# Kernel tuning notes

Measured on AMD Instinct MI355X. Metric: run time of the kernel, lower is better.

The kernel has to match this reference:

```python
import jax, jax.numpy as jnp
import numpy as np

B, N, D = 2, 2048, 1024
H = 16
HD = D // H  # head_dim = 64
EPS = 1e-5


def _layernorm(x, gamma, beta):
    mu = jnp.mean(x, axis=-1, keepdims=True)
    var = jnp.var(x, axis=-1, keepdims=True)
    return (x - mu) * jax.lax.rsqrt(var + EPS) * gamma + beta


def setup_inputs() -> dict:
    key = jax.random.key(0)
    ks = jax.random.split(key, 13)
    s = 1.0 / np.sqrt(D)
    return {
        "query": jax.random.normal(ks[0], (B, N, D), dtype=jnp.float32),
        "Wq": jax.random.uniform(ks[1], (D, D), jnp.float32, -s, s),
        "bq": jax.random.uniform(ks[2], (D,), jnp.float32, -s, s),
        "Wk": jax.random.uniform(ks[3], (D, D), jnp.float32, -s, s),
        "bk": jax.random.uniform(ks[4], (D,), jnp.float32, -s, s),
        "Wv": jax.random.uniform(ks[5], (D, D), jnp.float32, -s, s),
        "bv": jax.random.uniform(ks[6], (D,), jnp.float32, -s, s),
        "Wp": jax.random.uniform(ks[7], (D, D), jnp.float32, -s, s),
        "bp": jax.random.uniform(ks[8], (D,), jnp.float32, -s, s),
        "q_gamma": jnp.ones((HD,), jnp.float32),
        "q_beta": jnp.zeros((HD,), jnp.float32),
        "k_gamma": jnp.ones((HD,), jnp.float32),
        "k_beta": jnp.zeros((HD,), jnp.float32),
    }


def reference(query, Wq, bq, Wk, bk, Wv, bv, Wp, bp, q_gamma, q_beta, k_gamma, k_beta):
    # Linear projections (torch Linear: x @ W.T + b)
    def split_heads(x):  # [B,N,D] -> [B,H,N,HD]
        return x.reshape(B, N, H, HD).transpose(0, 2, 1, 3)

    Q = split_heads(query @ Wq.T + bq)
    K = split_heads(query @ Wk.T + bk)
    V = split_heads(query @ Wv.T + bv)

    # per-head QK LayerNorm
    Q = _layernorm(Q, q_gamma, q_beta)
    K = _layernorm(K, k_gamma, k_beta)

    scale = 1.0 / np.sqrt(HD)
    attn = jax.nn.softmax(jnp.einsum('bhqd,bhkd->bhqk', Q, K) * scale, axis=-1)
    # dropout_prob = 0.0 -> identity
    out = jnp.einsum('bhqk,bhkd->bqhd', attn, V).reshape(B, N, D)
    return out @ Wp.T + bp
```

## Files before the change

kernel.cpp:

```cpp
#include <hip/hip_runtime.h>
#include <math.h>

#define Bb 2
#define Nn 2048
#define Dd 1024
#define Hh 16
#define HD 64

typedef __attribute__((ext_vector_type(8))) short short8;
typedef __attribute__((ext_vector_type(4))) short short4v;
typedef __attribute__((ext_vector_type(4))) float floatx4;

__device__ __forceinline__ short f2bf(float x) {
    unsigned u = __float_as_uint(x);
    u += 0x7fffu + ((u >> 16) & 1u);
    return (short)(u >> 16);
}

#if defined(__has_builtin)
#  if __has_builtin(__builtin_amdgcn_mfma_f32_16x16x16bf16_1k)
#    define MFMA16(a, b, c) __builtin_amdgcn_mfma_f32_16x16x16bf16_1k(a, b, c, 0, 0, 0)
#  endif
#endif
#ifndef MFMA16
static __device__ __forceinline__ floatx4 mfma16_asm(short4v a, short4v b, floatx4 c) {
    asm volatile("v_mfma_f32_16x16x16_bf16 %0, %1, %2, %0" : "+v"(c) : "v"(a), "v"(b));
    return c;
}
#  define MFMA16(a, b, c) mfma16_asm(a, b, c)
#endif

__device__ __forceinline__ void gload16(const void* g, void* l) {
    __builtin_amdgcn_global_load_lds(
        (const __attribute__((address_space(1))) unsigned int*)g,
        (__attribute__((address_space(3))) unsigned int*)l,
        16, 0, 0);
}

#define QSCALE 0.18033688011112042f

__global__ __launch_bounds__(256) void cast_all(
    const float* __restrict__ x,
    const float* __restrict__ Wq, const float* __restrict__ Wk,
    const float* __restrict__ Wv, const float* __restrict__ Wp,
    short* __restrict__ xh, short* __restrict__ Wqh, short* __restrict__ Wkh,
    short* __restrict__ Wvh, short* __restrict__ Wph)
{
    const float* src; short* dst; int n4;
    switch (blockIdx.y) {
        case 0:  src = x;  dst = xh;  n4 = (Bb * Nn * Dd) / 4; break;
        case 1:  src = Wq; dst = Wqh; n4 = (Dd * Dd) / 4; break;
        case 2:  src = Wk; dst = Wkh; n4 = (Dd * Dd) / 4; break;
        case 3:  src = Wv; dst = Wvh; n4 = (Dd * Dd) / 4; break;
        default: src = Wp; dst = Wph; n4 = (Dd * Dd) / 4; break;
    }
    const int i = blockIdx.x * 256 + threadIdx.x;
    if (i >= n4) return;
    float4 v = ((const float4*)src)[i];
    short4v o;
    o.x = f2bf(v.x); o.y = f2bf(v.y); o.z = f2bf(v.z); o.w = f2bf(v.w);
    ((short4v*)dst)[i] = o;
}

__global__ __launch_bounds__(256) void qkv_ln_gemm(
    const short* __restrict__ xh,
    const short* __restrict__ Wqh, const short* __restrict__ Wkh,
    const short* __restrict__ Wvh,
    const float* __restrict__ bq, const float* __restrict__ bk,
    const float* __restrict__ bv,
    const float* __restrict__ qg, const float* __restrict__ qb,
    const float* __restrict__ kg, const float* __restrict__ kb,
    short* __restrict__ Qh, short* __restrict__ Kh, short* __restrict__ Vt)
{
    const int z = blockIdx.z;
    const short* A; const short* W;
    int rowBase, colBase, Nc;
    if (z < 2) { A = xh;  W = z ? Wkh : Wqh;
                 rowBase = blockIdx.x * 128; colBase = blockIdx.y * 128; Nc = Dd; }
    else       { A = Wvh; W = xh;
                 rowBase = blockIdx.y * 128; colBase = blockIdx.x * 128; Nc = Bb * Nn; }

    __shared__ __align__(16) short As[128 * 32];
    __shared__ __align__(16) short Ws[128 * 32];

    const int t    = threadIdx.x;
    const int w    = t >> 6;
    const int lane = t & 63;
    const int quad = lane >> 4;
    const int l15  = lane & 15;
    const int wy   = w >> 1;
    const int wx   = w & 1;

    const int r0 = t >> 2;
    const int kg4 = (t & 3) * 8;
    const short* aP = A + (size_t)(rowBase + r0) * Dd + kg4;
    const short* wP = W + (size_t)(colBase + r0) * Dd + kg4;
    const size_t rowskip = (size_t)64 * Dd;

    floatx4 acc[4][4];
    #pragma unroll
    for (int mi = 0; mi < 4; ++mi)
        #pragma unroll
        for (int ni = 0; ni < 4; ++ni)
            acc[mi][ni] = (floatx4){0.f, 0.f, 0.f, 0.f};

    for (int k0 = 0; k0 < Dd; k0 += 32) {
        gload16(aP,           &As[t * 8]);
        gload16(aP + rowskip, &As[(t + 256) * 8]);
        gload16(wP,           &Ws[t * 8]);
        gload16(wP + rowskip, &Ws[(t + 256) * 8]);
        aP += 32; wP += 32;
        __syncthreads();

        short8 af[4], bfr[4];
        #pragma unroll
        for (int i = 0; i < 4; ++i) {
            af[i]  = *(const short8*)&As[(wy * 64 + i * 16 + l15) * 32 + quad * 8];
            bfr[i] = *(const short8*)&Ws[(wx * 64 + i * 16 + l15) * 32 + quad * 8];
        }
        #pragma unroll
        for (int mi = 0; mi < 4; ++mi)
            #pragma unroll
            for (int ni = 0; ni < 4; ++ni)
                acc[mi][ni] = __builtin_amdgcn_mfma_f32_16x16x32_bf16(
                    af[mi], bfr[ni], acc[mi][ni], 0, 0, 0);
        __syncthreads();
    }

    if (z == 2) {
        #pragma unroll
        for (int mi = 0; mi < 4; ++mi) {
            #pragma unroll
            for (int r = 0; r < 4; ++r) {
                const size_t row = rowBase + wy * 64 + mi * 16 + quad * 4 + r;
                const float brv = bv[row];
                #pragma unroll
                for (int ni = 0; ni < 4; ++ni) {
                    const int col = colBase + wx * 64 + ni * 16 + l15;
                    Vt[row * (size_t)Nc + col] = f2bf(acc[mi][ni][r] + brv);
                }
            }
        }
    } else {
        const float* bias = z ? bk : bq;
        const float* gam  = z ? kg : qg;
        const float* bet  = z ? kb : qb;
        const float oscale = z ? 1.0f : QSCALE;
        short* out = z ? Kh : Qh;
        float bcol[4], g4[4], be4[4];
        #pragma unroll
        for (int ni = 0; ni < 4; ++ni) {
            const int ch = ni * 16 + l15;
            bcol[ni] = bias[colBase + wx * 64 + ch];
            g4[ni]   = gam[ch];
            be4[ni]  = bet[ch];
        }
        #pragma unroll
        for (int mi = 0; mi < 4; ++mi) {
            #pragma unroll
            for (int r = 0; r < 4; ++r) {
                const size_t row = rowBase + wy * 64 + mi * 16 + quad * 4 + r;
                float v[4], s = 0.f, s2 = 0.f;
                #pragma unroll
                for (int ni = 0; ni < 4; ++ni) {
                    v[ni] = acc[mi][ni][r] + bcol[ni];
                    s += v[ni]; s2 += v[ni] * v[ni];
                }
                #pragma unroll
                for (int d = 1; d < 16; d <<= 1) {
                    s  += __shfl_xor(s,  d, 16);
                    s2 += __shfl_xor(s2, d, 16);
                }
                const float mean = s * (1.0f / 64.0f);
                const float var  = s2 * (1.0f / 64.0f) - mean * mean;
                const float rr   = rsqrtf(var + 1e-5f);
                #pragma unroll
                for (int ni = 0; ni < 4; ++ni) {
                    const int col = colBase + wx * 64 + ni * 16 + l15;
                    out[row * (size_t)Dd + col] =
                        f2bf(((v[ni] - mean) * rr * g4[ni] + be4[ni]) * oscale);
                }
            }
        }
    }
}

__global__ __launch_bounds__(256) void gemm_mfma(
    const short* __restrict__ A, const short* __restrict__ W,
    const float* __restrict__ bias, float* __restrict__ Cf,
    int M, int K, int Nc)
{
    __shared__ __align__(16) short As[128 * 32];
    __shared__ __align__(16) short Ws[128 * 32];

    const int t    = threadIdx.x;
    const int w    = t >> 6;
    const int lane = t & 63;
    const int quad = lane >> 4;
    const int l15  = lane & 15;
    const int wy   = w >> 1;
    const int wx   = w & 1;
    const int rowBase = blockIdx.y * 128;
    const int colBase = blockIdx.x * 128;

    const int r0 = t >> 2;
    const int kg4 = (t & 3) * 8;
    const short* aP = A + (size_t)(rowBase + r0) * K + kg4;
    const short* wP = W + (size_t)(colBase + r0) * K + kg4;
    const size_t rowskip = (size_t)64 * K;

    floatx4 acc[4][4];
    #pragma unroll
    for (int mi = 0; mi < 4; ++mi)
        #pragma unroll
        for (int ni = 0; ni < 4; ++ni)
            acc[mi][ni] = (floatx4){0.f, 0.f, 0.f, 0.f};

    for (int k0 = 0; k0 < K; k0 += 32) {
        gload16(aP,           &As[t * 8]);
        gload16(aP + rowskip, &As[(t + 256) * 8]);
        gload16(wP,           &Ws[t * 8]);
        gload16(wP + rowskip, &Ws[(t + 256) * 8]);
        aP += 32; wP += 32;
        __syncthreads();

        short8 af[4], bfr[4];
        #pragma unroll
        for (int i = 0; i < 4; ++i) {
            af[i]  = *(const short8*)&As[(wy * 64 + i * 16 + l15) * 32 + quad * 8];
            bfr[i] = *(const short8*)&Ws[(wx * 64 + i * 16 + l15) * 32 + quad * 8];
        }
        #pragma unroll
        for (int mi = 0; mi < 4; ++mi)
            #pragma unroll
            for (int ni = 0; ni < 4; ++ni)
                acc[mi][ni] = __builtin_amdgcn_mfma_f32_16x16x32_bf16(
                    af[mi], bfr[ni], acc[mi][ni], 0, 0, 0);
        __syncthreads();
    }

    #pragma unroll
    for (int mi = 0; mi < 4; ++mi) {
        #pragma unroll
        for (int r = 0; r < 4; ++r) {
            const size_t row = rowBase + wy * 64 + mi * 16 + quad * 4 + r;
            #pragma unroll
            for (int ni = 0; ni < 4; ++ni) {
                const int col = colBase + wx * 64 + ni * 16 + l15;
                Cf[row * Nc + col] = acc[mi][ni][r] + bias[col];
            }
        }
    }
}

__global__ __launch_bounds__(256, 2) void flash_mfma(
    const short* __restrict__ Qh, const short* __restrict__ Kh,
    const short* __restrict__ Vt, short* __restrict__ ctx)
{
    const int qt = blockIdx.x;
    const int h  = blockIdx.y;
    const int b  = blockIdx.z;

    const int t    = threadIdx.x;
    const int w    = t >> 6;
    const int lane = t & 63;
    const int quad = lane >> 4;
    const int l15  = lane & 15;

    __shared__ __align__(16) short Ksh[64][72];
    __shared__ __align__(16) short Vsh[64][72];

    const size_t bhead = (size_t)b * Nn * Dd + (size_t)h * HD;

    short8 qf[2][2];
    #pragma unroll
    for (int qs = 0; qs < 2; ++qs) {
        const short* qp = Qh + bhead
            + (size_t)(qt * 128 + w * 32 + qs * 16 + l15) * Dd + quad * 8;
        qf[qs][0] = *(const short8*)qp;
        qf[qs][1] = *(const short8*)(qp + 32);
    }

    floatx4 accO[2][4], accL[2];
    #pragma unroll
    for (int qs = 0; qs < 2; ++qs) {
        #pragma unroll
        for (int n = 0; n < 4; ++n) accO[qs][n] = (floatx4){0.f, 0.f, 0.f, 0.f};
        accL[qs] = (floatx4){0.f, 0.f, 0.f, 0.f};
    }
    short4v ones;
    ones[0] = ones[1] = ones[2] = ones[3] = (short)0x3F80;

    const int s3  = t >> 3;
    const int c3  = ((t & 7) + (s3 & 7)) & 7;
    const int skg = c3 * 8;
    const short* kP = Kh + bhead + (size_t)s3 * Dd + skg;
    const short* vP = Vt + (size_t)(h * 64 + s3) * (Bb * Nn) + (size_t)b * Nn + skg;

    short8 kr0 = *(const short8*)kP;
    short8 kr1 = *(const short8*)(kP + 32 * Dd);
    short8 vr0 = *(const short8*)vP;
    short8 vr1 = *(const short8*)(vP + 32 * (Bb * Nn));

    for (int k0 = 0; k0 < Nn; k0 += 64) {
        *(short8*)&Ksh[s3][skg]      = kr0;
        *(short8*)&Ksh[s3 + 32][skg] = kr1;
        *(short8*)&Vsh[s3][skg]      = vr0;
        *(short8*)&Vsh[s3 + 32][skg] = vr1;
        __syncthreads();

        kP += 64 * Dd; vP += 64;
        kr0 = *(const short8*)kP;
        kr1 = *(const short8*)(kP + 32 * Dd);
        vr0 = *(const short8*)vP;
        vr1 = *(const short8*)(vP + 32 * (Bb * Nn));

        floatx4 accS[2][4];
        #pragma unroll
        for (int n = 0; n < 4; ++n) {
            short8 kf0 = *(const short8*)&Ksh[n * 16 + l15][quad * 8];
            short8 kf1 = *(const short8*)&Ksh[n * 16 + l15][32 + quad * 8];
            #pragma unroll
            for (int qs = 0; qs < 2; ++qs) {
                floatx4 zz = (floatx4){0.f, 0.f, 0.f, 0.f};
                zz = __builtin_amdgcn_mfma_f32_16x16x32_bf16(kf0, qf[qs][0], zz, 0, 0, 0);
                zz = __builtin_amdgcn_mfma_f32_16x16x32_bf16(kf1, qf[qs][1], zz, 0, 0, 0);
                accS[qs][n] = zz;
            }
        }

        short4v pfrag[2][4];
        #pragma unroll
        for (int qs = 0; qs < 2; ++qs) {
            #pragma unroll
            for (int n = 0; n < 4; ++n) {
                const unsigned u0 = __float_as_uint(exp2f(accS[qs][n][0]));
                const unsigned u1 = __float_as_uint(exp2f(accS[qs][n][1]));
                const unsigned u2 = __float_as_uint(exp2f(accS[qs][n][2]));
                const unsigned u3 = __float_as_uint(exp2f(accS[qs][n][3]));
                union { uint2 u; short4v s; } pk;
                pk.u.x = __builtin_amdgcn_perm(u1, u0, 0x07060302u);
                pk.u.y = __builtin_amdgcn_perm(u3, u2, 0x07060302u);
                pfrag[qs][n] = pk.s;
                accL[qs] = MFMA16(pk.s, ones, accL[qs]);
            }
        }

        #pragma unroll
        for (int n = 0; n < 4; ++n) {
            #pragma unroll
            for (int c = 0; c < 4; ++c) {
                const short4v vb =
                    *(const short4v*)&Vsh[c * 16 + l15][n * 16 + quad * 4];
                accO[0][c] = MFMA16(pfrag[0][n], vb, accO[0][c]);
                accO[1][c] = MFMA16(pfrag[1][n], vb, accO[1][c]);
            }
        }
        __syncthreads();
    }

    #pragma unroll
    for (int qs = 0; qs < 2; ++qs) {
        #pragma unroll
        for (int r = 0; r < 4; ++r) {
            const float lr = 1.0f / accL[qs][r];
            short* dst = ctx + (size_t)((b * Nn) + qt * 128 + w * 32 + qs * 16
                                        + quad * 4 + r) * Dd + h * HD + l15;
            #pragma unroll
            for (int n = 0; n < 4; ++n) dst[n * 16] = f2bf(accO[qs][n][r] * lr);
        }
    }
}

extern "C" void kernel_launch(void* const* d_in, const int* in_sizes, int n_in,
                              void* d_out, int out_size, void* d_ws, size_t ws_size,
                              hipStream_t stream) {
    const float* x   = (const float*)d_in[0];
    const float* Wq  = (const float*)d_in[1];
    const float* bq  = (const float*)d_in[2];
    const float* Wk  = (const float*)d_in[3];
    const float* bk  = (const float*)d_in[4];
    const float* Wv  = (const float*)d_in[5];
    const float* bv  = (const float*)d_in[6];
    const float* Wp  = (const float*)d_in[7];
    const float* bp  = (const float*)d_in[8];
    const float* qg  = (const float*)d_in[9];
    const float* qb  = (const float*)d_in[10];
    const float* kg  = (const float*)d_in[11];
    const float* kb  = (const float*)d_in[12];
    float* out = (float*)d_out;

    const size_t S = (size_t)Bb * Nn * Dd;
    short* wsb = (short*)d_ws;
    short* xh   = wsb;
    short* Vt   = wsb + S;
    short* Kh   = wsb + 2 * S;
    short* Qh   = wsb + 3 * S;
    short* ctxh = wsb + 4 * S;
    short* Wqh  = wsb + 5 * S;
    short* Wkh  = Wqh + Dd * Dd;
    short* Wvh  = Wkh + Dd * Dd;
    short* Wph  = Wvh + Dd * Dd;

    const int M = Bb * Nn;

    cast_all<<<dim3(4096, 5), 256, 0, stream>>>(x, Wq, Wk, Wv, Wp,
                                                xh, Wqh, Wkh, Wvh, Wph);

    qkv_ln_gemm<<<dim3(M / 128, Dd / 128, 3), 256, 0, stream>>>(
        xh, Wqh, Wkh, Wvh, bq, bk, bv, qg, qb, kg, kb, Qh, Kh, Vt);

    flash_mfma<<<dim3(Nn / 128, Hh, Bb), 256, 0, stream>>>(Qh, Kh, Vt, ctxh);

    gemm_mfma<<<dim3(Dd / 128, M / 128, 1), 256, 0, stream>>>(
        ctxh, Wph, bp, out, M, Dd, Dd);
}
```

Before: 238.4 us.

## Double-buffer K/V tiles in flash kernel and halve block size

```diff
diff --git a/kernel.cpp b/kernel.cpp
--- a/kernel.cpp
+++ b/kernel.cpp
@@ -253,7 +253,7 @@
     }
 }
 
-__global__ __launch_bounds__(256, 2) void flash_mfma(
+__global__ __launch_bounds__(128, 4) void flash_mfma(
     const short* __restrict__ Qh, const short* __restrict__ Kh,
     const short* __restrict__ Vt, short* __restrict__ ctx)
 {
@@ -267,8 +267,8 @@
     const int quad = lane >> 4;
     const int l15  = lane & 15;
 
-    __shared__ __align__(16) short Ksh[64][72];
-    __shared__ __align__(16) short Vsh[64][72];
+    __shared__ __align__(16) short Ksh[2][64][72];
+    __shared__ __align__(16) short Vsh[2][64][72];
 
     const size_t bhead = (size_t)b * Nn * Dd + (size_t)h * HD;
 
@@ -276,7 +276,7 @@
     #pragma unroll
     for (int qs = 0; qs < 2; ++qs) {
         const short* qp = Qh + bhead
-            + (size_t)(qt * 128 + w * 32 + qs * 16 + l15) * Dd + quad * 8;
+            + (size_t)(qt * 64 + w * 32 + qs * 16 + l15) * Dd + quad * 8;
         qf[qs][0] = *(const short8*)qp;
         qf[qs][1] = *(const short8*)(qp + 32);
     }
@@ -297,29 +297,35 @@
     const short* kP = Kh + bhead + (size_t)s3 * Dd + skg;
     const short* vP = Vt + (size_t)(h * 64 + s3) * (Bb * Nn) + (size_t)b * Nn + skg;
 
-    short8 kr0 = *(const short8*)kP;
-    short8 kr1 = *(const short8*)(kP + 32 * Dd);
-    short8 vr0 = *(const short8*)vP;
-    short8 vr1 = *(const short8*)(vP + 32 * (Bb * Nn));
-
+    short8 kr[4], vr[4];
+    #pragma unroll
+    for (int i = 0; i < 4; ++i) {
+        kr[i] = *(const short8*)(kP + (size_t)(16 * i) * Dd);
+        vr[i] = *(const short8*)(vP + (size_t)(16 * i) * (Bb * Nn));
+    }
+    #pragma unroll
+    for (int i = 0; i < 4; ++i) {
+        *(short8*)&Ksh[0][s3 + 16 * i][skg] = kr[i];
+        *(short8*)&Vsh[0][s3 + 16 * i][skg] = vr[i];
+    }
+    kP += 64 * Dd; vP += 64;
+
+    int cur = 0;
     for (int k0 = 0; k0 < Nn; k0 += 64) {
-        *(short8*)&Ksh[s3][skg]      = kr0;
-        *(short8*)&Ksh[s3 + 32][skg] = kr1;
-        *(short8*)&Vsh[s3][skg]      = vr0;
-        *(short8*)&Vsh[s3 + 32][skg] = vr1;
         __syncthreads();
 
+        #pragma unroll
+        for (int i = 0; i < 4; ++i) {
+            kr[i] = *(const short8*)(kP + (size_t)(16 * i) * Dd);
+            vr[i] = *(const short8*)(vP + (size_t)(16 * i) * (Bb * Nn));
+        }
         kP += 64 * Dd; vP += 64;
-        kr0 = *(const short8*)kP;
-        kr1 = *(const short8*)(kP + 32 * Dd);
-        vr0 = *(const short8*)vP;
-        vr1 = *(const short8*)(vP + 32 * (Bb * Nn));
 
         floatx4 accS[2][4];
         #pragma unroll
         for (int n = 0; n < 4; ++n) {
-            short8 kf0 = *(const short8*)&Ksh[n * 16 + l15][quad * 8];
-            short8 kf1 = *(const short8*)&Ksh[n * 16 + l15][32 + quad * 8];
+            short8 kf0 = *(const short8*)&Ksh[cur][n * 16 + l15][quad * 8];
+            short8 kf1 = *(const short8*)&Ksh[cur][n * 16 + l15][32 + quad * 8];
             #pragma unroll
             for (int qs = 0; qs < 2; ++qs) {
                 floatx4 zz = (floatx4){0.f, 0.f, 0.f, 0.f};
@@ -351,12 +357,18 @@
             #pragma unroll
             for (int c = 0; c < 4; ++c) {
                 const short4v vb =
-                    *(const short4v*)&Vsh[c * 16 + l15][n * 16 + quad * 4];
+                    *(const short4v*)&Vsh[cur][c * 16 + l15][n * 16 + quad * 4];
                 accO[0][c] = MFMA16(pfrag[0][n], vb, accO[0][c]);
                 accO[1][c] = MFMA16(pfrag[1][n], vb, accO[1][c]);
             }
         }
-        __syncthreads();
+
+        #pragma unroll
+        for (int i = 0; i < 4; ++i) {
+            *(short8*)&Ksh[cur ^ 1][s3 + 16 * i][skg] = kr[i];
+            *(short8*)&Vsh[cur ^ 1][s3 + 16 * i][skg] = vr[i];
+        }
+        cur ^= 1;
     }
 
     #pragma unroll
@@ -364,7 +376,7 @@
         #pragma unroll
         for (int r = 0; r < 4; ++r) {
             const float lr = 1.0f / accL[qs][r];
-            short* dst = ctx + (size_t)((b * Nn) + qt * 128 + w * 32 + qs * 16
+            short* dst = ctx + (size_t)((b * Nn) + qt * 64 + w * 32 + qs * 16
                                         + quad * 4 + r) * Dd + h * HD + l15;
             #pragma unroll
             for (int n = 0; n < 4; ++n) dst[n * 16] = f2bf(accO[qs][n][r] * lr);
@@ -410,7 +422,7 @@
     qkv_ln_gemm<<<dim3(M / 128, Dd / 128, 3), 256, 0, stream>>>(
         xh, Wqh, Wkh, Wvh, bq, bk, bv, qg, qb, kg, kb, Qh, Kh, Vt);
 
-    flash_mfma<<<dim3(Nn / 128, Hh, Bb), 256, 0, stream>>>(Qh, Kh, Vt, ctxh);
+    flash_mfma<<<dim3(Nn / 64, Hh, Bb), 128, 0, stream>>>(Qh, Kh, Vt, ctxh);
 
     gemm_mfma<<<dim3(Dd / 128, M / 128, 1), 256, 0, stream>>>(
         ctxh, Wph, bp, out, M, Dd, Dd);
```

New measurement: 242.5 us. Within noise of the previous version (+1.7%).
